# Kernel optimization log

Measured on AMD Instinct MI355X. Metric: run time of the kernel, lower is better.

The kernel has to match this reference:

```python
import jax, jax.numpy as jnp
import numpy as np
from jax import lax

PAD_IDX = 0
SOS_IDX = 1


def gru_cell(x, h, w_ih, w_hh, b_ih, b_hh):
    # PyTorch GRU cell: gates ordered [r, z, n]
    gi = x @ w_ih.T + b_ih            # [B, 3H]
    gh = h @ w_hh.T + b_hh            # [B, 3H]
    i_r, i_z, i_n = jnp.split(gi, 3, axis=-1)
    h_r, h_z, h_n = jnp.split(gh, 3, axis=-1)
    r = jax.nn.sigmoid(i_r + h_r)
    z = jax.nn.sigmoid(i_z + h_z)
    n = jnp.tanh(i_n + r * h_n)
    return (1.0 - z) * n + z * h


def setup_inputs() -> dict:
    key = jax.random.key(0)
    ks = jax.random.split(key, 24)
    B, S, T = 32, 64, 48
    Vs, Vt, E, H = 32000, 32000, 512, 1024
    sH = 1.0 / np.sqrt(H)
    sE = 1.0 / np.sqrt(E)

    def p(k, shape, scale):
        return jax.random.normal(k, shape, jnp.float32) * scale

    inp = {
        'source_ids': jax.random.randint(ks[0], (B, S), 0, Vs),
        'target_ids': jax.random.randint(ks[1], (B, T), 0, Vt),
        'enc_embed': p(ks[2], (Vs, E), 0.02).at[PAD_IDX].set(0.0),
        'enc_w_ih': p(ks[3], (3 * H, E), sE),
        'enc_w_hh': p(ks[4], (3 * H, H), sH),
        'enc_b_ih': p(ks[5], (3 * H,), sH),
        'enc_b_hh': p(ks[6], (3 * H,), sH),
        'wq': p(ks[7], (H, H), sH),
        'bq': p(ks[8], (H,), sH),
        'wk': p(ks[9], (H, H), sH),
        'bk': p(ks[10], (H,), sH),
        'ws': p(ks[11], (H,), sH),
        'bs': p(ks[12], (), sH),
        'dec_embed': p(ks[13], (Vt, E), 0.02).at[PAD_IDX].set(0.0),
        'dec_w_ih': p(ks[14], (3 * H, E + H), sH),
        'dec_w_hh': p(ks[15], (3 * H, H), sH),
        'dec_b_ih': p(ks[16], (3 * H,), sH),
        'dec_b_hh': p(ks[17], (3 * H,), sH),
        'wo': p(ks[18], (Vt, H), sH),
        'bo': p(ks[19], (Vt,), sH),
    }
    return inp


def reference(source_ids, target_ids, enc_embed, enc_w_ih, enc_w_hh, enc_b_ih,
              enc_b_hh, wq, bq, wk, bk, ws, bs, dec_embed, dec_w_ih, dec_w_hh,
              dec_b_ih, dec_b_hh, wo, bo):
    B, S = source_ids.shape
    T = target_ids.shape[1]
    H = wq.shape[0]

    # ----- encoder GRU -----
    enc_emb = enc_embed[source_ids]                  # [B,S,E] (dropout = identity, eval)
    h0 = jnp.zeros((B, H), enc_emb.dtype)

    def enc_step(h, x):
        h = gru_cell(x, h, enc_w_ih, enc_w_hh, enc_b_ih, enc_b_hh)
        return h, h

    h_final, enc_out = lax.scan(enc_step, h0, enc_emb.transpose(1, 0, 2))
    enc_out = enc_out.transpose(1, 0, 2)             # [B,S,H]

    mask = source_ids != PAD_IDX                     # [B,S]
    keys_proj = enc_out @ wk.T + bk                  # [B,S,H] (hoisted; linear, step-invariant)

    # ----- decoder with teacher forcing (ratio=1.0 => always teacher) -----
    dec_in = jnp.concatenate(
        [jnp.full((B, 1), SOS_IDX, dtype=target_ids.dtype), target_ids[:, 1:T - 1]],
        axis=1)                                      # [B,T-1]
    dec_emb = dec_embed[dec_in].transpose(1, 0, 2)   # [T-1,B,E]

    def dec_step(h, emb):
        q = h @ wq.T + bq                            # [B,H]
        scores = jnp.tanh(q[:, None, :] + keys_proj) @ ws + bs   # [B,S]
        scores = jnp.where(mask, scores, -jnp.inf)
        w = jax.nn.softmax(scores, axis=-1)          # [B,S]
        ctx = jnp.einsum('bs,bsh->bh', w, enc_out)   # [B,H]
        x = jnp.concatenate([emb, ctx], axis=-1)     # [B,E+H]
        h2 = gru_cell(x, h, dec_w_ih, dec_w_hh, dec_b_ih, dec_b_hh)
        logits = h2 @ wo.T + bo                      # [B,V]
        return h2, (logits, w)

    _, (logits, attn) = lax.scan(dec_step, h_final, dec_emb)
    logits = logits.transpose(1, 0, 2)               # [B,T-1,V]
    attn = attn.transpose(1, 0, 2)                   # [B,T-1,S]
    return logits, attn
```

## Files before the change

### kernel.cpp

```cpp
#include <hip/hip_runtime.h>


#define BB 32
#define SS 64
#define TT 48
#define TD 47
#define EE 512
#define HH 1024
#define GG 3072
#define VV 32000
#define SOS_IDX 1
#define MPAD 1536

typedef float f32x4 __attribute__((ext_vector_type(4)));
typedef short bf16x8 __attribute__((ext_vector_type(8)));

static __device__ __forceinline__ float sigmoid_f(float x) {
    return 1.0f / (1.0f + __expf(-x));
}
static __device__ __forceinline__ float tanh_f(float x) {
    return 1.0f - 2.0f / (__expf(2.0f * x) + 1.0f);
}
static __device__ __forceinline__ unsigned short f2bf(float f) {
    unsigned u = __float_as_uint(f);
    u = u + 0x7fffu + ((u >> 16) & 1u);
    return (unsigned short)(u >> 16);
}

__global__ void k_dec_idx(const int* __restrict__ tgt, int* __restrict__ idx) {
    int m = blockIdx.x * 256 + threadIdx.x;
    if (m < TD * BB) {
        int t = m >> 5, b = m & 31;
        idx[m] = (t == 0) ? SOS_IDX : tgt[b * TT + t];
    }
}

__global__ __launch_bounds__(256) void k_gemm128(
    const float* __restrict__ A, const float* __restrict__ Wt,
    const float* __restrict__ bias, float* __restrict__ C,
    const int* __restrict__ rowidx,
    int M, int N, int K, int lda, int ldw, int ldc)
{
    __shared__ __align__(16) float As[16][128];
    __shared__ __align__(16) float Bs[16][128];
    const int tid = threadIdx.x;
    const int tm = tid >> 4, tn = tid & 15;
    const int row0 = blockIdx.y * 128;
    const int col0 = blockIdx.x * 128;
    const int lr = tid >> 1;
    const int lq = tid & 1;

    long arow_off = -1;
    {
        int arow = row0 + lr;
        if (arow < M) {
            int r = rowidx ? rowidx[arow] : arow;
            arow_off = (long)r * lda;
        }
    }
    const long wrow_off = (long)(col0 + lr) * ldw;

    float acc[8][8];
#pragma unroll
    for (int i = 0; i < 8; ++i)
#pragma unroll
        for (int j = 0; j < 8; ++j) acc[i][j] = 0.f;

    for (int k0 = 0; k0 < K; k0 += 16) {
        f32x4 av0 = {0.f,0.f,0.f,0.f}, av1 = {0.f,0.f,0.f,0.f};
        if (arow_off >= 0) {
            av0 = *(const f32x4*)(A + arow_off + k0 + lq * 8);
            av1 = *(const f32x4*)(A + arow_off + k0 + lq * 8 + 4);
        }
        f32x4 wv0 = *(const f32x4*)(Wt + wrow_off + k0 + lq * 8);
        f32x4 wv1 = *(const f32x4*)(Wt + wrow_off + k0 + lq * 8 + 4);
        __syncthreads();
#pragma unroll
        for (int i = 0; i < 4; ++i) {
            As[lq * 8 + i][lr] = av0[i];
            As[lq * 8 + 4 + i][lr] = av1[i];
            Bs[lq * 8 + i][lr] = wv0[i];
            Bs[lq * 8 + 4 + i][lr] = wv1[i];
        }
        __syncthreads();
#pragma unroll
        for (int kk = 0; kk < 16; ++kk) {
            f32x4 a0 = *(const f32x4*)&As[kk][tm * 4];
            f32x4 a1 = *(const f32x4*)&As[kk][64 + tm * 4];
            f32x4 b0 = *(const f32x4*)&Bs[kk][tn * 4];
            f32x4 b1 = *(const f32x4*)&Bs[kk][64 + tn * 4];
            float a[8], b[8];
#pragma unroll
            for (int i = 0; i < 4; ++i) {
                a[i] = a0[i]; a[4 + i] = a1[i];
                b[i] = b0[i]; b[4 + i] = b1[i];
            }
#pragma unroll
            for (int i = 0; i < 8; ++i)
#pragma unroll
                for (int j = 0; j < 8; ++j) acc[i][j] += a[i] * b[j];
        }
    }

    f32x4 bv0 = {0.f,0.f,0.f,0.f}, bv1 = {0.f,0.f,0.f,0.f};
    if (bias) {
        bv0 = *(const f32x4*)(bias + col0 + tn * 4);
        bv1 = *(const f32x4*)(bias + col0 + 64 + tn * 4);
    }
#pragma unroll
    for (int i = 0; i < 8; ++i) {
        int m = row0 + ((i < 4) ? (tm * 4 + i) : (64 + tm * 4 + i - 4));
        if (m >= M) continue;
        f32x4 v0, v1;
#pragma unroll
        for (int j = 0; j < 4; ++j) {
            v0[j] = acc[i][j] + bv0[j];
            v1[j] = acc[i][4 + j] + bv1[j];
        }
        *(f32x4*)(C + (long)m * ldc + col0 + tn * 4) = v0;
        *(f32x4*)(C + (long)m * ldc + col0 + 64 + tn * 4) = v1;
    }
}

__global__ __launch_bounds__(256) void k_cvtA(
    const float* __restrict__ A, unsigned short* __restrict__ Ah,
    unsigned short* __restrict__ Al)
{
    size_t i4 = ((size_t)blockIdx.x * 256 + threadIdx.x) * 4;
    int row = (int)(i4 >> 10);
    f32x4 v = {0.f, 0.f, 0.f, 0.f};
    if (row < TD * BB) v = *(const f32x4*)(A + i4);
    ushort4 h, l;
    float hf;
    h.x = f2bf(v.x); hf = __uint_as_float((unsigned)h.x << 16); l.x = f2bf(v.x - hf);
    h.y = f2bf(v.y); hf = __uint_as_float((unsigned)h.y << 16); l.y = f2bf(v.y - hf);
    h.z = f2bf(v.z); hf = __uint_as_float((unsigned)h.z << 16); l.z = f2bf(v.z - hf);
    h.w = f2bf(v.w); hf = __uint_as_float((unsigned)h.w << 16); l.w = f2bf(v.w - hf);
    *(ushort4*)(Ah + i4) = h;
    *(ushort4*)(Al + i4) = l;
}

__global__ __launch_bounds__(256) void k_cvtB(
    const float* __restrict__ Bsrc, unsigned short* __restrict__ Bh)
{
    size_t i4 = ((size_t)blockIdx.x * 256 + threadIdx.x) * 4;
    f32x4 v = *(const f32x4*)(Bsrc + i4);
    ushort4 h;
    h.x = f2bf(v.x); h.y = f2bf(v.y); h.z = f2bf(v.z); h.w = f2bf(v.w);
    *(ushort4*)(Bh + i4) = h;
}

__global__ __launch_bounds__(256) void k_mfma_logits(
    const unsigned short* __restrict__ Ah,
    const unsigned short* __restrict__ Bh,
    const float* __restrict__ bo, float* __restrict__ C)
{
    __shared__ __align__(16) unsigned short As[128 * 64];
    __shared__ __align__(16) unsigned short Bs[128 * 64];
    const int tid = threadIdx.x;
    const int m0 = blockIdx.x * 128;
    const int n0 = blockIdx.y * 128;
    const int r = tid >> 1, half = tid & 1;
    const int lane = tid & 63, wid = tid >> 6;
    const int wm = wid >> 1, wn = wid & 1;

    f32x4 acc[4][4];
#pragma unroll
    for (int i = 0; i < 4; ++i)
#pragma unroll
        for (int j = 0; j < 4; ++j) acc[i][j] = (f32x4){0.f, 0.f, 0.f, 0.f};

    char* AsB = (char*)As;
    char* BsB = (char*)Bs;
    const int lwb = r * 128 + half * 64;
    const int swz = (r & 7) << 4;

    for (int kt = 0; kt < 32; ++kt) {
        const int kb = (kt & 15) * 64;
        const unsigned short* Ap = Ah + ((kt >> 4) ? (size_t)MPAD * 1024 : 0)
                                 + (size_t)(m0 + r) * 1024 + kb + half * 32;
        const unsigned short* Bp = Bh + (size_t)(n0 + r) * 1024 + kb + half * 32;
        f32x4 a0 = *(const f32x4*)(Ap + 0);
        f32x4 a1 = *(const f32x4*)(Ap + 8);
        f32x4 a2 = *(const f32x4*)(Ap + 16);
        f32x4 a3 = *(const f32x4*)(Ap + 24);
        f32x4 b0 = *(const f32x4*)(Bp + 0);
        f32x4 b1 = *(const f32x4*)(Bp + 8);
        f32x4 b2 = *(const f32x4*)(Bp + 16);
        f32x4 b3 = *(const f32x4*)(Bp + 24);
        __syncthreads();
        *(f32x4*)(AsB + ((lwb + 0)  ^ swz)) = a0;
        *(f32x4*)(AsB + ((lwb + 16) ^ swz)) = a1;
        *(f32x4*)(AsB + ((lwb + 32) ^ swz)) = a2;
        *(f32x4*)(AsB + ((lwb + 48) ^ swz)) = a3;
        *(f32x4*)(BsB + ((lwb + 0)  ^ swz)) = b0;
        *(f32x4*)(BsB + ((lwb + 16) ^ swz)) = b1;
        *(f32x4*)(BsB + ((lwb + 32) ^ swz)) = b2;
        *(f32x4*)(BsB + ((lwb + 48) ^ swz)) = b3;
        __syncthreads();
#pragma unroll
        for (int ks = 0; ks < 2; ++ks) {
            bf16x8 af[4], bf[4];
#pragma unroll
            for (int u = 0; u < 4; ++u) {
                int ml = wm * 64 + u * 16 + (lane & 15);
                int byteA = ml * 128 + ks * 64 + ((lane >> 4) << 4);
                af[u] = *(const bf16x8*)(AsB + (byteA ^ ((ml & 7) << 4)));
                int nl = wn * 64 + u * 16 + (lane & 15);
                int byteB = nl * 128 + ks * 64 + ((lane >> 4) << 4);
                bf[u] = *(const bf16x8*)(BsB + (byteB ^ ((nl & 7) << 4)));
            }
#pragma unroll
            for (int mi = 0; mi < 4; ++mi)
#pragma unroll
                for (int ni = 0; ni < 4; ++ni)
                    acc[mi][ni] = __builtin_amdgcn_mfma_f32_16x16x32_bf16(
                        af[mi], bf[ni], acc[mi][ni], 0, 0, 0);
        }
    }

    const int cl = lane & 15, rq = lane >> 4;
#pragma unroll
    for (int ni = 0; ni < 4; ++ni) {
        int col = n0 + wn * 64 + ni * 16 + cl;
        float bias = bo[col];
#pragma unroll
        for (int mi = 0; mi < 4; ++mi) {
#pragma unroll
            for (int j = 0; j < 4; ++j) {
                int m = m0 + wm * 64 + mi * 16 + rq * 4 + j;
                if (m < TD * BB) {
                    int orow = (m & 31) * TD + (m >> 5);
                    C[(size_t)orow * VV + col] = acc[mi][ni][j] + bias;
                }
            }
        }
    }
}

__global__ __launch_bounds__(512, 2) void k_enc_step(
    const float* __restrict__ gi, const float* __restrict__ Whh,
    const float* __restrict__ bhh, float* __restrict__ enc_out, int s)
{
    __shared__ float red[12][16][32];
    __shared__ float sums[12][32];
    const int tid = threadIdx.x, bid = blockIdx.x;
    const int b = tid & 31, ks = tid >> 5;
    const int j0 = bid * 4;
    const int kc = ks * 64;

    float acc[12];
#pragma unroll
    for (int u = 0; u < 12; ++u) acc[u] = 0.f;
    if (s > 0) {
        f32x4 hreg[16];
        const float* hb = enc_out + ((size_t)b * SS + (s - 1)) * HH + kc;
#pragma unroll
        for (int i = 0; i < 16; ++i) hreg[i] = *(const f32x4*)(hb + (i << 2));
#pragma unroll
        for (int jj = 0; jj < 4; ++jj) {
            const float* pr = Whh + ((size_t)(j0 + jj) << 10) + kc;
            const float* pz = Whh + ((size_t)(HH + j0 + jj) << 10) + kc;
            const float* pn = Whh + ((size_t)(2 * HH + j0 + jj) << 10) + kc;
            float ar = 0.f, az = 0.f, an = 0.f;
#pragma unroll
            for (int i = 0; i < 16; ++i) {
                f32x4 h4 = hreg[i];
                f32x4 w;
                w = *(const f32x4*)(pr + (i << 2));
                ar += h4.x * w.x + h4.y * w.y + h4.z * w.z + h4.w * w.w;
                w = *(const f32x4*)(pz + (i << 2));
                az += h4.x * w.x + h4.y * w.y + h4.z * w.z + h4.w * w.w;
                w = *(const f32x4*)(pn + (i << 2));
                an += h4.x * w.x + h4.y * w.y + h4.z * w.z + h4.w * w.w;
            }
            acc[jj] = ar; acc[4 + jj] = az; acc[8 + jj] = an;
        }
    }
#pragma unroll
    for (int u = 0; u < 12; ++u) red[u][ks][b] = acc[u];
    __syncthreads();
    if (tid < 384) {
        int u = tid >> 5, fb = tid & 31;
        float x = 0.f;
#pragma unroll
        for (int q = 0; q < 16; ++q) x += red[u][q][fb];
        sums[u][fb] = x;
    }
    __syncthreads();
    if (tid < 32) {
        const f32x4 bh0 = *(const f32x4*)(bhh + j0);
        const f32x4 bh1 = *(const f32x4*)(bhh + HH + j0);
        const f32x4 bh2 = *(const f32x4*)(bhh + 2 * HH + j0);
        const float* gr = gi + (size_t)(tid * SS + s) * GG;
        f32x4 g0 = *(const f32x4*)(gr + j0);
        f32x4 g1 = *(const f32x4*)(gr + HH + j0);
        f32x4 g2 = *(const f32x4*)(gr + 2 * HH + j0);
        f32x4 hold = {0.f, 0.f, 0.f, 0.f};
        if (s > 0) hold = *(const f32x4*)(enc_out + ((size_t)tid * SS + (s - 1)) * HH + j0);
        f32x4 hn;
#pragma unroll
        for (int e = 0; e < 4; ++e) {
            float r = sigmoid_f(g0[e] + sums[e][tid] + bh0[e]);
            float z = sigmoid_f(g1[e] + sums[4 + e][tid] + bh1[e]);
            float n = tanh_f(g2[e] + r * (sums[8 + e][tid] + bh2[e]));
            hn[e] = (1.f - z) * n + z * hold[e];
        }
        *(f32x4*)(enc_out + ((size_t)tid * SS + s) * HH + j0) = hn;
    }
}

__global__ __launch_bounds__(512, 2) void k_hq(
    const float* __restrict__ hbase, long hstride,
    const float* __restrict__ Whh, const float* __restrict__ wq,
    const float* __restrict__ bq, float* __restrict__ qbuf,
    float* __restrict__ hsums)
{
    __shared__ float red[16][16][32];
    __shared__ float qsum[4][32];
    const int tid = threadIdx.x, bid = blockIdx.x;
    const int b = tid & 31, ks = tid >> 5;
    const int j0 = bid * 4;
    const int kc = ks * 64;

    f32x4 hreg[16];
    const float* hb = hbase + (size_t)b * hstride + kc;
#pragma unroll
    for (int i = 0; i < 16; ++i) hreg[i] = *(const f32x4*)(hb + (i << 2));
    float acc[16];
#pragma unroll
    for (int jj = 0; jj < 4; ++jj) {
        const float* pr = Whh + ((size_t)(j0 + jj) << 10) + kc;
        const float* pz = Whh + ((size_t)(HH + j0 + jj) << 10) + kc;
        const float* pn = Whh + ((size_t)(2 * HH + j0 + jj) << 10) + kc;
        const float* pq = wq + ((size_t)(j0 + jj) << 10) + kc;
        float ar = 0.f, az = 0.f, an = 0.f, aq = 0.f;
#pragma unroll
        for (int i = 0; i < 16; ++i) {
            f32x4 h4 = hreg[i];
            f32x4 w;
            w = *(const f32x4*)(pr + (i << 2));
            ar += h4.x * w.x + h4.y * w.y + h4.z * w.z + h4.w * w.w;
            w = *(const f32x4*)(pz + (i << 2));
            az += h4.x * w.x + h4.y * w.y + h4.z * w.z + h4.w * w.w;
            w = *(const f32x4*)(pn + (i << 2));
            an += h4.x * w.x + h4.y * w.y + h4.z * w.z + h4.w * w.w;
            w = *(const f32x4*)(pq + (i << 2));
            aq += h4.x * w.x + h4.y * w.y + h4.z * w.z + h4.w * w.w;
        }
        acc[jj] = ar; acc[4 + jj] = az; acc[8 + jj] = an; acc[12 + jj] = aq;
    }
#pragma unroll
    for (int u = 0; u < 16; ++u) red[u][ks][b] = acc[u];
    __syncthreads();
    {
        int u = tid >> 5, fb = tid & 31;
        float x = 0.f;
#pragma unroll
        for (int q = 0; q < 16; ++q) x += red[u][q][fb];
        if (u < 12) {
            int g = u >> 2, jj = u & 3;
            hsums[(size_t)g * BB * HH + (size_t)fb * HH + j0 + jj] = x;
        } else {
            qsum[u - 12][fb] = x;
        }
    }
    __syncthreads();
    if (tid < 32) {
        const f32x4 bq4 = *(const f32x4*)(bq + j0);
        f32x4 qv;
        qv.x = qsum[0][tid] + bq4.x;
        qv.y = qsum[1][tid] + bq4.y;
        qv.z = qsum[2][tid] + bq4.z;
        qv.w = qsum[3][tid] + bq4.w;
        *(f32x4*)(qbuf + (size_t)tid * HH + j0) = qv;
    }
}

__global__ __launch_bounds__(512, 2) void k_attn_fin(
    const float* __restrict__ qbuf, const float* __restrict__ keys,
    const float* __restrict__ wsv, const float* __restrict__ bsv,
    const int* __restrict__ src, const float* __restrict__ encproj,
    const float* __restrict__ gi, const float* __restrict__ bhh,
    const float* __restrict__ hsums, const float* __restrict__ hbase,
    long hstride, float* __restrict__ h2all, float* __restrict__ attn_out,
    int t)
{
    __shared__ float qs[HH];
    __shared__ float wss[HH];
    __shared__ float sc[8][64];
    __shared__ float wl[64];
    __shared__ float xls[GG];
    const int ab = blockIdx.x;
    const int tid = threadIdx.x;
    if (tid < 256) {
        *(f32x4*)&qs[tid * 4] = *(const f32x4*)(qbuf + (size_t)ab * HH + tid * 4);
        *(f32x4*)&wss[tid * 4] = *(const f32x4*)(wsv + tid * 4);
    }
    __syncthreads();
    {
        const int s4 = tid >> 3, kq = tid & 7;
        const float* kr = keys + (size_t)(ab * SS + s4) * HH + kq * 128;
        float a = 0.f;
        for (int i = 0; i < 32; ++i) {
            f32x4 kv = *(const f32x4*)(kr + (i << 2));
            int k = kq * 128 + (i << 2);
            a += tanh_f(qs[k] + kv.x) * wss[k]
               + tanh_f(qs[k + 1] + kv.y) * wss[k + 1]
               + tanh_f(qs[k + 2] + kv.z) * wss[k + 2]
               + tanh_f(qs[k + 3] + kv.w) * wss[k + 3];
        }
        sc[kq][s4] = a;
    }
    __syncthreads();
    if (tid < 64) {
        float v = bsv[0];
#pragma unroll
        for (int q = 0; q < 8; ++q) v += sc[q][tid];
        bool valid = src[ab * SS + tid] != 0;
        float m = valid ? v : -3.0e38f;
        for (int off = 32; off; off >>= 1) m = fmaxf(m, __shfl_xor(m, off));
        float e = valid ? __expf(v - m) : 0.f;
        float ssum = e;
        for (int off = 32; off; off >>= 1) ssum += __shfl_xor(ssum, off);
        float wgt = e / ssum;
        wl[tid] = wgt;
        attn_out[((size_t)ab * TD + t) * SS + tid] = wgt;
    }
    __syncthreads();
    {
        float xa[6] = {0.f, 0.f, 0.f, 0.f, 0.f, 0.f};
        for (int s2 = 0; s2 < SS; ++s2) {
            float wgt = wl[s2];
            const float* ep = encproj + (size_t)(ab * SS + s2) * GG;
#pragma unroll
            for (int u = 0; u < 6; ++u)
                xa[u] += wgt * ep[u * 512 + tid];
        }
#pragma unroll
        for (int u = 0; u < 6; ++u) xls[u * 512 + tid] = xa[u];
    }
    __syncthreads();
    const float* gr = gi + (size_t)(t * BB + ab) * GG;
#pragma unroll
    for (int half = 0; half < 2; ++half) {
        int j = half * 512 + tid;
        float g0 = gr[j] + xls[j];
        float g1 = gr[HH + j] + xls[HH + j];
        float g2 = gr[2 * HH + j] + xls[2 * HH + j];
        float sh0 = hsums[(size_t)0 * BB * HH + (size_t)ab * HH + j];
        float sh1 = hsums[(size_t)1 * BB * HH + (size_t)ab * HH + j];
        float sh2 = hsums[(size_t)2 * BB * HH + (size_t)ab * HH + j];
        float r = sigmoid_f(g0 + sh0 + bhh[j]);
        float z = sigmoid_f(g1 + sh1 + bhh[HH + j]);
        float n = tanh_f(g2 + r * (sh2 + bhh[2 * HH + j]));
        float hold = hbase[(size_t)ab * hstride + j];
        h2all[((size_t)t * BB + ab) * HH + j] = (1.f - z) * n + z * hold;
    }
}

extern "C" void kernel_launch(void* const* d_in, const int* in_sizes, int n_in,
                              void* d_out, int out_size, void* d_ws, size_t ws_size,
                              hipStream_t stream)
{
    const int*   src  = (const int*)d_in[0];
    const int*   tgt  = (const int*)d_in[1];
    const float* eemb = (const float*)d_in[2];
    const float* ewih = (const float*)d_in[3];
    const float* ewhh = (const float*)d_in[4];
    const float* ebih = (const float*)d_in[5];
    const float* ebhh = (const float*)d_in[6];
    const float* wq   = (const float*)d_in[7];
    const float* bq   = (const float*)d_in[8];
    const float* wk   = (const float*)d_in[9];
    const float* bk   = (const float*)d_in[10];
    const float* wsv  = (const float*)d_in[11];
    const float* bsv  = (const float*)d_in[12];
    const float* demb = (const float*)d_in[13];
    const float* dwih = (const float*)d_in[14];
    const float* dwhh = (const float*)d_in[15];
    const float* dbih = (const float*)d_in[16];
    const float* dbhh = (const float*)d_in[17];
    const float* wo   = (const float*)d_in[18];
    const float* bo   = (const float*)d_in[19];
    float* out = (float*)d_out;

    float* w = (float*)d_ws;
    float* enc_gi  = w;
    float* dec_gi  = enc_gi  + (size_t)BB * SS * GG;
    float* enc_out = dec_gi  + (size_t)TD * BB * GG;
    float* keys    = enc_out + (size_t)BB * SS * HH;
    float* h2all   = keys    + (size_t)BB * SS * HH;
    float* qbuf    = h2all   + (size_t)TD * BB * HH;
    float* hsums   = qbuf    + (size_t)BB * HH;
    int*   didx    = (int*)(hsums + (size_t)3 * BB * HH);
    unsigned short* Ah = (unsigned short*)(didx + TD * BB + 32);
    unsigned short* Al = Ah + (size_t)MPAD * 1024;
    unsigned short* Bh = (unsigned short*)w;

    float* encproj = enc_gi;
    float* attn_out = out + (size_t)BB * TD * VV;

    k_dec_idx<<<dim3((TD * BB + 255) / 256), 256, 0, stream>>>(tgt, didx);

    k_gemm128<<<dim3(GG / 128, (BB * SS) / 128), 256, 0, stream>>>(
        eemb, ewih, ebih, enc_gi, src, BB * SS, GG, EE, EE, EE, GG);
    k_gemm128<<<dim3(GG / 128, (TD * BB + 127) / 128), 256, 0, stream>>>(
        demb, dwih, dbih, dec_gi, didx, TD * BB, GG, EE, EE, EE + HH, GG);

    for (int s = 0; s < SS; ++s)
        k_enc_step<<<dim3(256), dim3(512), 0, stream>>>(
            enc_gi, ewhh, ebhh, enc_out, s);

    k_gemm128<<<dim3(HH / 128, (BB * SS) / 128), 256, 0, stream>>>(
        enc_out, wk, bk, keys, nullptr, BB * SS, HH, HH, HH, HH, HH);
    k_gemm128<<<dim3(GG / 128, (BB * SS) / 128), 256, 0, stream>>>(
        enc_out, dwih + EE, nullptr, encproj, nullptr,
        BB * SS, GG, HH, HH, EE + HH, GG);

    for (int t = 0; t < TD; ++t) {
        const float* hbase = (t == 0) ? enc_out + (size_t)(SS - 1) * HH
                                      : h2all + (size_t)(t - 1) * BB * HH;
        long hstride = (t == 0) ? (long)SS * HH : (long)HH;
        k_hq<<<dim3(256), dim3(512), 0, stream>>>(
            hbase, hstride, dwhh, wq, bq, qbuf, hsums);
        k_attn_fin<<<dim3(BB), dim3(512), 0, stream>>>(
            qbuf, keys, wsv, bsv, src, encproj, dec_gi, dbhh, hsums,
            hbase, hstride, h2all, attn_out, t);
    }

    k_cvtA<<<dim3(MPAD * 1024 / 1024), 256, 0, stream>>>(h2all, Ah, Al);
    k_cvtB<<<dim3(VV * 1024 / 1024), 256, 0, stream>>>(wo, Bh);
    k_mfma_logits<<<dim3(MPAD / 128, VV / 128), 256, 0, stream>>>(
        Ah, Bh, bo, out);
}
```

Before: 4.494 ms.

## Split attention-finalize across two blocks per batch row; fuse hi/lo logits k-loop

The per-step attention/GRU finalize kernel now launches 64 blocks instead of 32, with each pair of blocks sharing a batch row and splitting the hidden columns in half. Each block still recomputes the full attention scores and softmax, which duplicates that work, but the context projection and gate arithmetic are halved per block and twice as many CUs take part. Separately, the logits MFMA kernel loads the hi and lo bf16 A-tiles into two LDS buffers in one k-iteration instead of walking 32 iterations. This halves the B-tile loads and barriers, at the cost of extra LDS and registers.

```diff
diff --git a/kernel.cpp b/kernel.cpp
--- a/kernel.cpp
+++ b/kernel.cpp
@@ -155,7 +155,8 @@
     const unsigned short* __restrict__ Bh,
     const float* __restrict__ bo, float* __restrict__ C)
 {
-    __shared__ __align__(16) unsigned short As[128 * 64];
+    __shared__ __align__(16) unsigned short As0[128 * 64];
+    __shared__ __align__(16) unsigned short As1[128 * 64];
     __shared__ __align__(16) unsigned short Bs[128 * 64];
     const int tid = threadIdx.x;
     const int m0 = blockIdx.x * 128;
@@ -170,52 +171,65 @@
 #pragma unroll
         for (int j = 0; j < 4; ++j) acc[i][j] = (f32x4){0.f, 0.f, 0.f, 0.f};
 
-    char* AsB = (char*)As;
-    char* BsB = (char*)Bs;
+    char* As0B = (char*)As0;
+    char* As1B = (char*)As1;
+    char* BsB  = (char*)Bs;
     const int lwb = r * 128 + half * 64;
     const int swz = (r & 7) << 4;
 
-    for (int kt = 0; kt < 32; ++kt) {
-        const int kb = (kt & 15) * 64;
-        const unsigned short* Ap = Ah + ((kt >> 4) ? (size_t)MPAD * 1024 : 0)
-                                 + (size_t)(m0 + r) * 1024 + kb + half * 32;
-        const unsigned short* Bp = Bh + (size_t)(n0 + r) * 1024 + kb + half * 32;
-        f32x4 a0 = *(const f32x4*)(Ap + 0);
-        f32x4 a1 = *(const f32x4*)(Ap + 8);
-        f32x4 a2 = *(const f32x4*)(Ap + 16);
-        f32x4 a3 = *(const f32x4*)(Ap + 24);
+    for (int kt = 0; kt < 16; ++kt) {
+        const int kb = kt * 64;
+        const unsigned short* Ap0 = Ah + (size_t)(m0 + r) * 1024 + kb + half * 32;
+        const unsigned short* Ap1 = Ap0 + (size_t)MPAD * 1024;
+        const unsigned short* Bp  = Bh + (size_t)(n0 + r) * 1024 + kb + half * 32;
+        f32x4 a0 = *(const f32x4*)(Ap0 + 0);
+        f32x4 a1 = *(const f32x4*)(Ap0 + 8);
+        f32x4 a2 = *(const f32x4*)(Ap0 + 16);
+        f32x4 a3 = *(const f32x4*)(Ap0 + 24);
+        f32x4 c0 = *(const f32x4*)(Ap1 + 0);
+        f32x4 c1 = *(const f32x4*)(Ap1 + 8);
+        f32x4 c2 = *(const f32x4*)(Ap1 + 16);
+        f32x4 c3 = *(const f32x4*)(Ap1 + 24);
         f32x4 b0 = *(const f32x4*)(Bp + 0);
         f32x4 b1 = *(const f32x4*)(Bp + 8);
         f32x4 b2 = *(const f32x4*)(Bp + 16);
         f32x4 b3 = *(const f32x4*)(Bp + 24);
         __syncthreads();
-        *(f32x4*)(AsB + ((lwb + 0)  ^ swz)) = a0;
-        *(f32x4*)(AsB + ((lwb + 16) ^ swz)) = a1;
-        *(f32x4*)(AsB + ((lwb + 32) ^ swz)) = a2;
-        *(f32x4*)(AsB + ((lwb + 48) ^ swz)) = a3;
-        *(f32x4*)(BsB + ((lwb + 0)  ^ swz)) = b0;
-        *(f32x4*)(BsB + ((lwb + 16) ^ swz)) = b1;
-        *(f32x4*)(BsB + ((lwb + 32) ^ swz)) = b2;
-        *(f32x4*)(BsB + ((lwb + 48) ^ swz)) = b3;
+        *(f32x4*)(As0B + ((lwb + 0)  ^ swz)) = a0;
+        *(f32x4*)(As0B + ((lwb + 16) ^ swz)) = a1;
+        *(f32x4*)(As0B + ((lwb + 32) ^ swz)) = a2;
+        *(f32x4*)(As0B + ((lwb + 48) ^ swz)) = a3;
+        *(f32x4*)(As1B + ((lwb + 0)  ^ swz)) = c0;
+        *(f32x4*)(As1B + ((lwb + 16) ^ swz)) = c1;
+        *(f32x4*)(As1B + ((lwb + 32) ^ swz)) = c2;
+        *(f32x4*)(As1B + ((lwb + 48) ^ swz)) = c3;
+        *(f32x4*)(BsB  + ((lwb + 0)  ^ swz)) = b0;
+        *(f32x4*)(BsB  + ((lwb + 16) ^ swz)) = b1;
+        *(f32x4*)(BsB  + ((lwb + 32) ^ swz)) = b2;
+        *(f32x4*)(BsB  + ((lwb + 48) ^ swz)) = b3;
         __syncthreads();
 #pragma unroll
         for (int ks = 0; ks < 2; ++ks) {
-            bf16x8 af[4], bf[4];
+            bf16x8 bf[4], af[4], ag[4];
 #pragma unroll
             for (int u = 0; u < 4; ++u) {
-                int ml = wm * 64 + u * 16 + (lane & 15);
-                int byteA = ml * 128 + ks * 64 + ((lane >> 4) << 4);
-                af[u] = *(const bf16x8*)(AsB + (byteA ^ ((ml & 7) << 4)));
                 int nl = wn * 64 + u * 16 + (lane & 15);
                 int byteB = nl * 128 + ks * 64 + ((lane >> 4) << 4);
                 bf[u] = *(const bf16x8*)(BsB + (byteB ^ ((nl & 7) << 4)));
+                int ml = wm * 64 + u * 16 + (lane & 15);
+                int byteA = ml * 128 + ks * 64 + ((lane >> 4) << 4);
+                af[u] = *(const bf16x8*)(As0B + (byteA ^ ((ml & 7) << 4)));
+                ag[u] = *(const bf16x8*)(As1B + (byteA ^ ((ml & 7) << 4)));
             }
 #pragma unroll
             for (int mi = 0; mi < 4; ++mi)
 #pragma unroll
-                for (int ni = 0; ni < 4; ++ni)
+                for (int ni = 0; ni < 4; ++ni) {
                     acc[mi][ni] = __builtin_amdgcn_mfma_f32_16x16x32_bf16(
                         af[mi], bf[ni], acc[mi][ni], 0, 0, 0);
+                    acc[mi][ni] = __builtin_amdgcn_mfma_f32_16x16x32_bf16(
+                        ag[mi], bf[ni], acc[mi][ni], 0, 0, 0);
+                }
         }
     }
 
@@ -390,8 +404,8 @@
     __shared__ float wss[HH];
     __shared__ float sc[8][64];
     __shared__ float wl[64];
-    __shared__ float xls[GG];
-    const int ab = blockIdx.x;
+    __shared__ float xls[3 * 512];
+    const int ab = blockIdx.x & 31, part = blockIdx.x >> 5;
     const int tid = threadIdx.x;
     if (tid < 256) {
         *(f32x4*)&qs[tid * 4] = *(const f32x4*)(qbuf + (size_t)ab * HH + tid * 4);
@@ -425,29 +439,30 @@
         for (int off = 32; off; off >>= 1) ssum += __shfl_xor(ssum, off);
         float wgt = e / ssum;
         wl[tid] = wgt;
-        attn_out[((size_t)ab * TD + t) * SS + tid] = wgt;
+        if (part == 0)
+            attn_out[((size_t)ab * TD + t) * SS + tid] = wgt;
     }
     __syncthreads();
     {
-        float xa[6] = {0.f, 0.f, 0.f, 0.f, 0.f, 0.f};
+        float xa[3] = {0.f, 0.f, 0.f};
+        const int colbase = part * 512 + tid;
         for (int s2 = 0; s2 < SS; ++s2) {
             float wgt = wl[s2];
-            const float* ep = encproj + (size_t)(ab * SS + s2) * GG;
-#pragma unroll
-            for (int u = 0; u < 6; ++u)
-                xa[u] += wgt * ep[u * 512 + tid];
-        }
-#pragma unroll
-        for (int u = 0; u < 6; ++u) xls[u * 512 + tid] = xa[u];
-    }
-    __syncthreads();
-    const float* gr = gi + (size_t)(t * BB + ab) * GG;
-#pragma unroll
-    for (int half = 0; half < 2; ++half) {
-        int j = half * 512 + tid;
-        float g0 = gr[j] + xls[j];
-        float g1 = gr[HH + j] + xls[HH + j];
-        float g2 = gr[2 * HH + j] + xls[2 * HH + j];
+            const float* ep = encproj + (size_t)(ab * SS + s2) * GG + colbase;
+#pragma unroll
+            for (int u = 0; u < 3; ++u)
+                xa[u] += wgt * ep[u * HH];
+        }
+#pragma unroll
+        for (int u = 0; u < 3; ++u) xls[u * 512 + tid] = xa[u];
+    }
+    __syncthreads();
+    {
+        const int j = part * 512 + tid;
+        const float* gr = gi + (size_t)(t * BB + ab) * GG;
+        float g0 = gr[j] + xls[tid];
+        float g1 = gr[HH + j] + xls[512 + tid];
+        float g2 = gr[2 * HH + j] + xls[1024 + tid];
         float sh0 = hsums[(size_t)0 * BB * HH + (size_t)ab * HH + j];
         float sh1 = hsums[(size_t)1 * BB * HH + (size_t)ab * HH + j];
         float sh2 = hsums[(size_t)2 * BB * HH + (size_t)ab * HH + j];
@@ -524,7 +539,7 @@
         long hstride = (t == 0) ? (long)SS * HH : (long)HH;
         k_hq<<<dim3(256), dim3(512), 0, stream>>>(
             hbase, hstride, dwhh, wq, bq, qbuf, hsums);
-        k_attn_fin<<<dim3(BB), dim3(512), 0, stream>>>(
+        k_attn_fin<<<dim3(64), dim3(512), 0, stream>>>(
             qbuf, keys, wsv, bsv, src, encproj, dec_gi, dbhh, hsums,
             hbase, hstride, h2all, attn_out, t);
     }
```

Result: faster. 3.984 ms (median of 2 runs) (-11.4%).
